# Optimization experiments

Hardware: AMD Instinct MI355X
Metric: run time of the kernel (lower is better)

## Reference

```python
import jax, jax.numpy as jnp
import numpy as np

N_HEAD = 16
SPARSE_TOPK = 64
NEG_INF = float('-inf')


def setup_inputs() -> dict:
    key = jax.random.key(0)
    ks = jax.random.split(key, 12)
    B, T, C = 4, 1024, 1024
    s = 0.02
    q = jax.random.normal(ks[0], (B, T, C), jnp.float32)
    kv = jax.random.normal(ks[1], (B, T, C), jnp.float32)  # forward asserts k == v
    tgt_mask = jnp.tril(jnp.ones((T, T), jnp.bool_)).reshape(1, 1, T, T)
    inp = {'q': q, 'k': kv, 'v': kv, 'tgt_mask': tgt_mask}
    for i, n in enumerate(['Wq', 'Wk', 'Wv', 'Wo']):
        inp[n] = jax.random.normal(ks[2 + i], (C, C), jnp.float32) * s
    for i, n in enumerate(['bq', 'bk', 'bv', 'bo']):
        inp[n] = jax.random.normal(ks[6 + i], (C,), jnp.float32) * s
    return inp


def reference(q, k, v, tgt_mask, Wq, Wk, Wv, Wo, bq, bk, bv, bo):
    B, T, C = q.shape
    H = N_HEAD
    hd = C // H
    scale = 1.0 / np.sqrt(hd).astype(np.float32)
    # QKV projections -> [B, H, T, hd]
    qh = (q @ Wq + bq).reshape(B, T, H, hd).transpose(0, 2, 1, 3)
    kh = (k @ Wk + bk).reshape(B, T, H, hd).transpose(0, 2, 1, 3)
    vh = (v @ Wv + bv).reshape(B, T, H, hd).transpose(0, 2, 1, 3)
    # full attention scores [B, H, T, T]
    att = jnp.einsum('bhtd,bhsd->bhts', qh, kh) * scale
    # causal mask: masked_fill where tgt_mask == 0
    att = jnp.where(tgt_mask[:, :, :T, :T], att, NEG_INF)
    # top-k sparse pruning: keep entries >= k-th largest per row (ties kept)
    top, _ = jax.lax.top_k(att, SPARSE_TOPK)
    vk = top[..., -1:]  # [B, H, T, 1]
    att = jnp.where(att < vk, NEG_INF, att)
    att = jax.nn.softmax(att, axis=-1)
    # dropout is identity in eval (p=0.0)
    y = jnp.einsum('bhts,bhsd->bhtd', att, vh)
    y = y.transpose(0, 2, 1, 3).reshape(B, T, C)
    return y @ Wo + bo
```

## Files before the change

kernel.cpp:

```cpp
#include <hip/hip_runtime.h>
#include <hip/hip_bf16.h>
#include <math.h>

typedef __attribute__((ext_vector_type(8))) short short8;
typedef __attribute__((ext_vector_type(4))) float f32x4;
typedef __attribute__((ext_vector_type(4))) int int4v;

#define SCL 0.1803368801111204f

static __device__ __forceinline__ unsigned short f2bf(float f) {
  unsigned u = __float_as_uint(f);
  u = u + 0x7FFFu + ((u >> 16) & 1u);
  return (unsigned short)(u >> 16);
}
static __device__ __forceinline__ unsigned pack2(float lo, float hi) {
  const unsigned ul = __float_as_uint(lo) + 0x8000u;
  const unsigned uh = __float_as_uint(hi) + 0x8000u;
  return (uh & 0xFFFF0000u) | (ul >> 16);
}

static __device__ __forceinline__ unsigned keyof(float x) {
  unsigned u = __float_as_uint(x);
  return (u & 0x80000000u) ? ~u : (u | 0x80000000u);
}
static __device__ __forceinline__ float keyinv(unsigned k) {
  unsigned u = (k & 0x80000000u) ? (k & 0x7FFFFFFFu) : ~k;
  return __uint_as_float(u);
}

static __device__ __forceinline__ int saddr(int r, int cc) {
  return (((r << 9) + cc) << 2) ^ ((r & 7) << 4);
}
static __device__ __forceinline__ int paddr(int r, int c) {
  return ((r << 11) + (c << 1)) ^ ((r & 7) << 4);
}

static __device__ __forceinline__ void gld_lds16(const unsigned short* g, unsigned short* l) {
  __builtin_amdgcn_global_load_lds(
      (const __attribute__((address_space(1))) void*)g,
      (__attribute__((address_space(3))) void*)l, 16, 0, 0);
}

__global__ __launch_bounds__(256) void wtrans4_k(const float* __restrict__ Wq,
                                                 const float* __restrict__ Wk,
                                                 const float* __restrict__ Wv,
                                                 const float* __restrict__ Wo,
                                                 unsigned short* __restrict__ Wqt,
                                                 unsigned short* __restrict__ Wkt,
                                                 unsigned short* __restrict__ Wvt,
                                                 unsigned short* __restrict__ Wot) {
  const int z = blockIdx.z;
  const float* W = (z == 0) ? Wq : (z == 1) ? Wk : (z == 2) ? Wv : Wo;
  unsigned short* Wt = (z == 0) ? Wqt : (z == 1) ? Wkt : (z == 2) ? Wvt : Wot;
  __shared__ float tile[32][33];
  const int tx = threadIdx.x, ty = threadIdx.y;
  const int x0 = blockIdx.x * 32, y0 = blockIdx.y * 32;
#pragma unroll
  for (int j = 0; j < 4; ++j)
    tile[ty + j * 8][tx] = W[(y0 + ty + j * 8) * 1024 + x0 + tx];
  __syncthreads();
#pragma unroll
  for (int j = 0; j < 4; ++j)
    Wt[(x0 + ty + j * 8) * 1024 + (y0 + tx)] = f2bf(tile[tx][ty + j * 8]);
}

template <int MODE>
static __device__ __forceinline__ void gemm_bodyF(unsigned short* As0, unsigned short* Bs0,
                                                  unsigned short* As1, unsigned short* Bs1,
                                                  const float* __restrict__ A,
                                                  const unsigned short* __restrict__ Bt,
                                                  const float* __restrict__ bias,
                                                  void* __restrict__ out) {
  const int tid = threadIdx.x;
  const int lane = tid & 63, w = tid >> 6;
  const int wr = w >> 1, wc = w & 1;
  const int m0 = blockIdx.y * 128, n0 = blockIdx.x * 128;
  const int l15 = lane & 15, l4 = lane >> 4;
  f32x4 acc[4][4] = {};
  const int r0 = tid >> 2, s0 = (tid & 3) * 8;
  const int r1 = r0 + 64;
  const float* gA0 = A + (m0 + r0) * 1024 + s0;
  const float* gA1 = A + (m0 + r1) * 1024 + s0;
  const unsigned short* gB0 = Bt + (n0 + r0) * 1024 + s0;
  const unsigned short* gB1 = Bt + (n0 + r1) * 1024 + s0;
  const int oA0 = r0 * 32 + s0, oA1 = r1 * 32 + s0;

  {
    const f32x4 a0 = *(const f32x4*)(gA0);
    const f32x4 a1 = *(const f32x4*)(gA0 + 4);
    const f32x4 c0 = *(const f32x4*)(gA1);
    const f32x4 c1 = *(const f32x4*)(gA1 + 4);
    gld_lds16(gB0, Bs0 + oA0);
    gld_lds16(gB1, Bs0 + oA1);
    int4v pa, pb;
    pa[0] = (int)pack2(a0[0], a0[1]); pa[1] = (int)pack2(a0[2], a0[3]);
    pa[2] = (int)pack2(a1[0], a1[1]); pa[3] = (int)pack2(a1[2], a1[3]);
    pb[0] = (int)pack2(c0[0], c0[1]); pb[1] = (int)pack2(c0[2], c0[3]);
    pb[2] = (int)pack2(c1[0], c1[1]); pb[3] = (int)pack2(c1[2], c1[3]);
    *(int4v*)(As0 + oA0) = pa;
    *(int4v*)(As0 + oA1) = pb;
  }
  __syncthreads();

  for (int kt = 0; kt < 32; ++kt) {
    f32x4 a0, a1, c0, c1;
    if (kt < 31) {
      const int k0n = (kt + 1) * 32;
      a0 = *(const f32x4*)(gA0 + k0n);
      a1 = *(const f32x4*)(gA0 + k0n + 4);
      c0 = *(const f32x4*)(gA1 + k0n);
      c1 = *(const f32x4*)(gA1 + k0n + 4);
      unsigned short* Bsn = (kt & 1) ? Bs0 : Bs1;
      gld_lds16(gB0 + k0n, Bsn + oA0);
      gld_lds16(gB1 + k0n, Bsn + oA1);
    }
    const unsigned short* Asc = (kt & 1) ? As1 : As0;
    const unsigned short* Bsc = (kt & 1) ? Bs1 : Bs0;
    short8 af[4], bfr[4];
#pragma unroll
    for (int i = 0; i < 4; ++i) {
      af[i]  = *(const short8*)(Asc + (wr * 64 + i * 16 + l15) * 32 + l4 * 8);
      bfr[i] = *(const short8*)(Bsc + (wc * 64 + i * 16 + l15) * 32 + l4 * 8);
    }
#pragma unroll
    for (int i = 0; i < 4; ++i)
#pragma unroll
      for (int j = 0; j < 4; ++j)
        acc[i][j] = __builtin_amdgcn_mfma_f32_16x16x32_bf16(af[i], bfr[j], acc[i][j], 0, 0, 0);
    if (kt < 31) {
      unsigned short* Asn = (kt & 1) ? As0 : As1;
      int4v pa, pb;
      pa[0] = (int)pack2(a0[0], a0[1]); pa[1] = (int)pack2(a0[2], a0[3]);
      pa[2] = (int)pack2(a1[0], a1[1]); pa[3] = (int)pack2(a1[2], a1[3]);
      pb[0] = (int)pack2(c0[0], c0[1]); pb[1] = (int)pack2(c0[2], c0[3]);
      pb[2] = (int)pack2(c1[0], c1[1]); pb[3] = (int)pack2(c1[2], c1[3]);
      *(int4v*)(Asn + oA0) = pa;
      *(int4v*)(Asn + oA1) = pb;
    }
    __syncthreads();
  }
#pragma unroll
  for (int i = 0; i < 4; ++i) {
#pragma unroll
    for (int j = 0; j < 4; ++j) {
      const int n = n0 + wc * 64 + j * 16 + l15;
      const float bv = bias[n];
#pragma unroll
      for (int r = 0; r < 4; ++r) {
        const int m = m0 + wr * 64 + i * 16 + l4 * 4 + r;
        const float v = acc[i][j][r] + bv;
        const int bb = m >> 10, t = m & 1023, hh = n >> 6, dd = n & 63;
        const unsigned short bfv = f2bf(v);
        if (MODE == 0)
          ((unsigned short*)out)[(((bb << 4) + hh) * 1024 + t) * 64 + dd] = bfv;
        else
          ((unsigned short*)out)[(((bb << 4) + hh) * 64 + dd) * 1024 + t] = bfv;
      }
    }
  }
}

__global__ __launch_bounds__(256) void gemm_qkv_k(
    const float* q, const float* k, const float* v,
    const unsigned short* Wqt, const unsigned short* Wkt, const unsigned short* Wvt,
    const float* bq, const float* bk, const float* bv,
    unsigned short* Qh, unsigned short* Kh, unsigned short* Vth) {
  __shared__ unsigned short As0[128 * 32], Bs0[128 * 32], As1[128 * 32], Bs1[128 * 32];
  const int z = blockIdx.z;
  const float* A           = (z == 0) ? q   : ((z == 1) ? k   : v);
  const unsigned short* Bt = (z == 0) ? Wqt : ((z == 1) ? Wkt : Wvt);
  const float* bias        = (z == 0) ? bq  : ((z == 1) ? bk  : bv);
  if (z == 2) gemm_bodyF<1>(As0, Bs0, As1, Bs1, A, Bt, bias, Vth);
  else        gemm_bodyF<0>(As0, Bs0, As1, Bs1, A, Bt, bias, z ? Kh : Qh);
}

__global__ __launch_bounds__(256) void gemm_out_k(const unsigned short* __restrict__ Y,
                                                  const unsigned short* __restrict__ Wot,
                                                  const float* __restrict__ bo,
                                                  float* __restrict__ out) {
  __shared__ unsigned short As0[128 * 32], Bs0[128 * 32], As1[128 * 32], Bs1[128 * 32];
  const int tid = threadIdx.x;
  const int lane = tid & 63, w = tid >> 6;
  const int wr = w >> 1, wc = w & 1;
  const int m0 = blockIdx.y * 128, n0 = blockIdx.x * 128;
  const int l15 = lane & 15, l4 = lane >> 4;
  f32x4 acc[4][4] = {};
  const int r0 = tid >> 2, s0 = (tid & 3) * 8;
  const int r1 = r0 + 64;
  const unsigned short* gA0 = Y + (m0 + r0) * 1024 + s0;
  const unsigned short* gA1 = Y + (m0 + r1) * 1024 + s0;
  const unsigned short* gB0 = Wot + (n0 + r0) * 1024 + s0;
  const unsigned short* gB1 = Wot + (n0 + r1) * 1024 + s0;
  const int oA0 = r0 * 32 + s0, oA1 = r1 * 32 + s0;

  gld_lds16(gA0, As0 + oA0);
  gld_lds16(gA1, As0 + oA1);
  gld_lds16(gB0, Bs0 + oA0);
  gld_lds16(gB1, Bs0 + oA1);
  __syncthreads();

  for (int kt = 0; kt < 32; ++kt) {
    if (kt < 31) {
      const int k0n = (kt + 1) * 32;
      unsigned short* Asn = (kt & 1) ? As0 : As1;
      unsigned short* Bsn = (kt & 1) ? Bs0 : Bs1;
      gld_lds16(gA0 + k0n, Asn + oA0);
      gld_lds16(gA1 + k0n, Asn + oA1);
      gld_lds16(gB0 + k0n, Bsn + oA0);
      gld_lds16(gB1 + k0n, Bsn + oA1);
    }
    const unsigned short* Asc = (kt & 1) ? As1 : As0;
    const unsigned short* Bsc = (kt & 1) ? Bs1 : Bs0;
    short8 af[4], bfr[4];
#pragma unroll
    for (int i = 0; i < 4; ++i) {
      af[i]  = *(const short8*)(Asc + (wr * 64 + i * 16 + l15) * 32 + l4 * 8);
      bfr[i] = *(const short8*)(Bsc + (wc * 64 + i * 16 + l15) * 32 + l4 * 8);
    }
#pragma unroll
    for (int i = 0; i < 4; ++i)
#pragma unroll
      for (int j = 0; j < 4; ++j)
        acc[i][j] = __builtin_amdgcn_mfma_f32_16x16x32_bf16(af[i], bfr[j], acc[i][j], 0, 0, 0);
    __syncthreads();
  }
#pragma unroll
  for (int i = 0; i < 4; ++i) {
#pragma unroll
    for (int j = 0; j < 4; ++j) {
      const int n = n0 + wc * 64 + j * 16 + l15;
      const float bv = bo[n];
#pragma unroll
      for (int r = 0; r < 4; ++r) {
        const int m = m0 + wr * 64 + i * 16 + l4 * 4 + r;
        out[m * 1024 + n] = acc[i][j][r] + bv;
      }
    }
  }
}

template <int NVAL, bool FORCE>
static __device__ __forceinline__ void process_row(char* __restrict__ smem, float (&v)[NVAL],
                                                   const int r, const int Lr, const int Lpad,
                                                   const int lane, float* __restrict__ RED2) {
  float lm = v[0];
#pragma unroll
  for (int i = 1; i < NVAL; ++i) lm = fmaxf(lm, v[i]);
  float mx = lm;
#pragma unroll
  for (int o = 32; o; o >>= 1) mx = fmaxf(mx, __shfl_xor(mx, o));

  float thr = -INFINITY;
  if (FORCE || Lr > 64) {
    float mn = lm;
#pragma unroll
    for (int o = 32; o; o >>= 1) mn = fminf(mn, __shfl_xor(mn, o));
    unsigned lo = (unsigned)__builtin_amdgcn_readfirstlane((int)keyof(mn));
    unsigned hi = (unsigned)__builtin_amdgcn_readfirstlane((int)keyof(mx)) + 1u;
    int cl = Lr, ch = 0, alt = 0;
    while (hi - lo > 1u) {
      const unsigned span = hi - lo;
      unsigned off;
      if (alt) off = span >> 1;
      else {
        const float fr = (float)(cl - 64) / (float)(cl - ch);
        off = (unsigned)(fr * (float)span);
        if (off < 1u) off = 1u;
        if (off > span - 1u) off = span - 1u;
      }
      alt ^= 1;
      const unsigned mid = lo + off;
      const float tm = keyinv(mid);
      int cnt = 0;
#pragma unroll
      for (int i = 0; i < NVAL; ++i) cnt += (int)__popcll(__ballot(v[i] >= tm));
      if (cnt >= 64) { lo = mid; cl = cnt; if (cnt == 64) break; }
      else { hi = mid; ch = cnt; }
    }
    thr = keyinv(lo);
  }

  float s = 0.f;
  unsigned pk[NVAL / 2];
#pragma unroll
  for (int p = 0; p < NVAL / 2; ++p) {
    const float p0 = (v[2 * p]     >= thr) ? exp2f(v[2 * p]     - mx) : 0.f;
    const float p1 = (v[2 * p + 1] >= thr) ? exp2f(v[2 * p + 1] - mx) : 0.f;
    s += p0 + p1;
    pk[p] = (unsigned)f2bf(p0) | ((unsigned)f2bf(p1) << 16);
  }
#pragma unroll
  for (int o = 32; o; o >>= 1) s += __shfl_xor(s, o);
  if (lane == 0) RED2[r] = 1.f / s;
#pragma unroll
  for (int p = 0; p < NVAL / 2; ++p) {
    const int c = ((p & 3) << 7) + (lane << 1) + ((p >= 4) ? 512 : 0);
    if (c < Lpad) *(unsigned*)(smem + paddr(r, c)) = pk[p];
  }
}

static __device__ __forceinline__ void pv_phase(char* __restrict__ smem,
                                                const unsigned short* __restrict__ Vh,
                                                unsigned short* __restrict__ Y,
                                                const int t0, const int h, const int b,
                                                const int lane, const int w, const int Lpad) {
  const int l15 = lane & 15, l4 = lane >> 4;
  float* RED  = (float*)(smem + 32768);
  float* RED2 = (float*)(smem + 32768 + 4352);
  const int nST = Lpad >> 5;
  const int stMid = (nST + 1) >> 1;
  const int d0 = (w & 3) * 16;
  const int stLo = (w < 4) ? 0 : stMid;
  const int stHi = (w < 4) ? stMid : nST;
  f32x4 acc = {0.f, 0.f, 0.f, 0.f};
  for (int st = stLo; st < stHi; ++st) {
    const int sb = st * 32 + l4 * 8;
    const short8 paf = *(const short8*)(smem + paddr(l15, sb));
    const short8 vb = *(const short8*)(Vh + (d0 + l15) * 1024 + sb);
    acc = __builtin_amdgcn_mfma_f32_16x16x32_bf16(paf, vb, acc, 0, 0, 0);
  }
  if (w >= 4) {
    const int base = (w - 4) * 272 + l15;
#pragma unroll
    for (int r = 0; r < 4; ++r) RED[base + (l4 * 4 + r) * 17] = acc[r];
  }
  __syncthreads();
  if (w < 4) {
    const int base = w * 272 + l15;
    const int d = (h << 6) + d0 + l15;
#pragma unroll
    for (int r = 0; r < 4; ++r) {
      const float inv = RED2[l4 * 4 + r];
      const float vr = (acc[r] + RED[base + (l4 * 4 + r) * 17]) * inv;
      const int tg = t0 + l4 * 4 + r;
      Y[((b << 10) + tg) * 1024 + d] = f2bf(vr);
    }
  }
}

__global__ __launch_bounds__(512, 6) void attn_hv_k(const unsigned short* __restrict__ Q,
                                                    const unsigned short* __restrict__ K,
                                                    const unsigned short* __restrict__ Vt,
                                                    unsigned short* __restrict__ Y) {
  extern __shared__ __align__(16) char smem[];
  const int tid = threadIdx.x, lane = tid & 63, w = tid >> 6;
  const int t0 = 1008 - 16 * (int)blockIdx.x;
  const int h = blockIdx.y, b = blockIdx.z;
  const unsigned short* Qp = Q + (((b * 16 + h) * 1024) + t0) * 64;
  const unsigned short* Kh = K + (b * 16 + h) * 65536;
  const unsigned short* Vh = Vt + (b * 16 + h) * 65536;
  const int L = t0 + 16;
  const int Lpad = (L + 31) & ~31;
  const int nCT = L >> 4;
  const int l15 = lane & 15, l4 = lane >> 4;
  float* RED2 = (float*)(smem + 32768 + 4352);

  const short8 aq0 = *(const short8*)(Qp + l15 * 64 + l4 * 8);
  const short8 aq1 = *(const short8*)(Qp + l15 * 64 + 32 + l4 * 8);

  auto qk_chunk = [&](int tlo, int thi) {
    for (int ct = tlo + w; ct < thi; ct += 8) {
      const int c0 = ct * 16;
      const short8 kb0 = *(const short8*)(Kh + (c0 + l15) * 64 + l4 * 8);
      const short8 kb1 = *(const short8*)(Kh + (c0 + l15) * 64 + 32 + l4 * 8);
      f32x4 acc = {0.f, 0.f, 0.f, 0.f};
      acc = __builtin_amdgcn_mfma_f32_16x16x32_bf16(aq0, kb0, acc, 0, 0, 0);
      acc = __builtin_amdgcn_mfma_f32_16x16x32_bf16(aq1, kb1, acc, 0, 0, 0);
      const int c = c0 + l15, cc = c & 511;
      if (ct == nCT - 1) {
#pragma unroll
        for (int r = 0; r < 4; ++r) {
          const int row = l4 * 4 + r;
          *(float*)(smem + saddr(row, cc)) = (c <= t0 + row) ? acc[r] * SCL : -INFINITY;
        }
      } else {
#pragma unroll
        for (int r = 0; r < 4; ++r)
          *(float*)(smem + saddr(l4 * 4 + r, cc)) = acc[r] * SCL;
      }
    }
  };

  qk_chunk(0, 32);
  __syncthreads();
  const int rA = w * 2, rB = rA + 1;
  const int LrA = t0 + rA + 1, LrB = t0 + rB + 1;
  float vA[16], vB[16];
#pragma unroll
  for (int p = 0; p < 4; ++p) {
    const int c = (p << 7) + (lane << 1);
    const float2 tA = *(const float2*)(smem + saddr(rA, c));
    const float2 tB = *(const float2*)(smem + saddr(rB, c));
    vA[2 * p] = tA.x; vA[2 * p + 1] = tA.y;
    vB[2 * p] = tB.x; vB[2 * p + 1] = tB.y;
  }
  __syncthreads();
  qk_chunk(32, nCT);
  __syncthreads();
#pragma unroll
  for (int p = 0; p < 4; ++p) {
    const int cc = (p << 7) + (lane << 1);
    const float2 tA = *(const float2*)(smem + saddr(rA, cc));
    const bool vld = (cc + 512) < L;
    vA[8 + 2 * p] = vld ? tA.x : -INFINITY;
    vA[9 + 2 * p] = vld ? tA.y : -INFINITY;
  }
  process_row<16, true>(smem, vA, rA, LrA, Lpad, lane, RED2);
#pragma unroll
  for (int p = 0; p < 4; ++p) {
    const int cc = (p << 7) + (lane << 1);
    const float2 tB = *(const float2*)(smem + saddr(rB, cc));
    const bool vld = (cc + 512) < L;
    vB[8 + 2 * p] = vld ? tB.x : -INFINITY;
    vB[9 + 2 * p] = vld ? tB.y : -INFINITY;
  }
  process_row<16, true>(smem, vB, rB, LrB, Lpad, lane, RED2);
  __syncthreads();
  pv_phase(smem, Vh, Y, t0, h, b, lane, w, Lpad);
}

__global__ __launch_bounds__(512, 6) void attn_lt_k(const unsigned short* __restrict__ Q,
                                                    const unsigned short* __restrict__ K,
                                                    const unsigned short* __restrict__ Vt,
                                                    unsigned short* __restrict__ Y) {
  extern __shared__ __align__(16) char smem[];
  const int tid = threadIdx.x, lane = tid & 63, w = tid >> 6;
  const int t0 = 496 - 16 * (int)blockIdx.x;
  const int h = blockIdx.y, b = blockIdx.z;
  const unsigned short* Qp = Q + (((b * 16 + h) * 1024) + t0) * 64;
  const unsigned short* Kh = K + (b * 16 + h) * 65536;
  const unsigned short* Vh = Vt + (b * 16 + h) * 65536;
  const int L = t0 + 16;
  const int Lpad = (L + 31) & ~31;
  const int nCT = L >> 4;
  const int l15 = lane & 15, l4 = lane >> 4;
  float* RED2 = (float*)(smem + 32768 + 4352);

  const short8 aq0 = *(const short8*)(Qp + l15 * 64 + l4 * 8);
  const short8 aq1 = *(const short8*)(Qp + l15 * 64 + 32 + l4 * 8);

  for (int ct = w; ct < nCT; ct += 8) {
    const int c0 = ct * 16;
    const short8 kb0 = *(const short8*)(Kh + (c0 + l15) * 64 + l4 * 8);
    const short8 kb1 = *(const short8*)(Kh + (c0 + l15) * 64 + 32 + l4 * 8);
    f32x4 acc = {0.f, 0.f, 0.f, 0.f};
    acc = __builtin_amdgcn_mfma_f32_16x16x32_bf16(aq0, kb0, acc, 0, 0, 0);
    acc = __builtin_amdgcn_mfma_f32_16x16x32_bf16(aq1, kb1, acc, 0, 0, 0);
    const int c = c0 + l15, cc = c & 511;
    if (ct == nCT - 1) {
#pragma unroll
      for (int r = 0; r < 4; ++r) {
        const int row = l4 * 4 + r;
        *(float*)(smem + saddr(row, cc)) = (c <= t0 + row) ? acc[r] * SCL : -INFINITY;
      }
    } else {
#pragma unroll
      for (int r = 0; r < 4; ++r)
        *(float*)(smem + saddr(l4 * 4 + r, cc)) = acc[r] * SCL;
    }
  }
  __syncthreads();

  const int rA = w * 2, rB = rA + 1;
  const int LrA = t0 + rA + 1, LrB = t0 + rB + 1;
  float vA[8], vB[8];
#pragma unroll
  for (int p = 0; p < 4; ++p) {
    const int c = (p << 7) + (lane << 1);
    const float2 tA = *(const float2*)(smem + saddr(rA, c));
    const float2 tB = *(const float2*)(smem + saddr(rB, c));
    const bool vld = c < L;
    vA[2 * p]     = vld ? tA.x : -INFINITY;
    vA[2 * p + 1] = vld ? tA.y : -INFINITY;
    vB[2 * p]     = vld ? tB.x : -INFINITY;
    vB[2 * p + 1] = vld ? tB.y : -INFINITY;
  }
  process_row<8, false>(smem, vA, rA, LrA, Lpad, lane, RED2);
  process_row<8, false>(smem, vB, rB, LrB, Lpad, lane, RED2);
  __syncthreads();
  pv_phase(smem, Vh, Y, t0, h, b, lane, w, Lpad);
}

extern "C" void kernel_launch(void* const* d_in, const int* in_sizes, int n_in,
                              void* d_out, int out_size, void* d_ws, size_t ws_size,
                              hipStream_t stream) {
  const float* q  = (const float*)d_in[0];
  const float* k  = (const float*)d_in[1];
  const float* v  = (const float*)d_in[2];
  const float* Wq = (const float*)d_in[4];
  const float* Wk = (const float*)d_in[5];
  const float* Wv = (const float*)d_in[6];
  const float* Wo = (const float*)d_in[7];
  const float* bq = (const float*)d_in[8];
  const float* bk = (const float*)d_in[9];
  const float* bv = (const float*)d_in[10];
  const float* bo = (const float*)d_in[11];

  char* ws = (char*)d_ws;
  const size_t MB = 1u << 20;
  unsigned short* Y   = (unsigned short*)(ws + 0 * MB);
  unsigned short* Wqt = (unsigned short*)(ws + 24 * MB);
  unsigned short* Wkt = (unsigned short*)(ws + 26 * MB);
  unsigned short* Wvt = (unsigned short*)(ws + 28 * MB);
  unsigned short* Wot = (unsigned short*)(ws + 30 * MB);
  unsigned short* Qh  = (unsigned short*)(ws + 32 * MB);
  unsigned short* Kh  = (unsigned short*)(ws + 40 * MB);
  unsigned short* Vth = (unsigned short*)(ws + 48 * MB);

  wtrans4_k<<<dim3(32, 32, 4), dim3(32, 8), 0, stream>>>(Wq, Wk, Wv, Wo, Wqt, Wkt, Wvt, Wot);
  gemm_qkv_k<<<dim3(8, 32, 3), 256, 0, stream>>>(q, k, v, Wqt, Wkt, Wvt,
                                                 bq, bk, bv, Qh, Kh, Vth);
  attn_hv_k<<<dim3(32, 16, 4), 512, 37248, stream>>>(Qh, Kh, Vth, Y);
  attn_lt_k<<<dim3(32, 16, 4), 512, 37248, stream>>>(Qh, Kh, Vth, Y);
  gemm_out_k<<<dim3(8, 32), 256, 0, stream>>>(Y, Wot, bo, (float*)d_out);
}
```

Before: 223.6 us.

## Double attention block size to 16 waves, one query row per wave

Both attention kernels now launch 1024 threads instead of 512. Each of the 16 waves handles one query row in the top-k/softmax phase instead of two. The PV phase splits the key dimension four ways instead of two, combining partial sums through a larger shared-memory reduction buffer. The goal is to cut the serial per-wave work in the row-processing and PV phases. In exchange it uses more shared memory per block and more barrier overhead, and the new launch bounds may limit registers and occupancy.

```diff
diff --git a/kernel.cpp b/kernel.cpp
--- a/kernel.cpp
+++ b/kernel.cpp
@@ -299,49 +299,51 @@
   }
 }
 
-static __device__ __forceinline__ void pv_phase(char* __restrict__ smem,
-                                                const unsigned short* __restrict__ Vh,
-                                                unsigned short* __restrict__ Y,
-                                                const int t0, const int h, const int b,
-                                                const int lane, const int w, const int Lpad) {
+static __device__ __forceinline__ void pv_phase16(char* __restrict__ smem,
+                                                  const unsigned short* __restrict__ Vh,
+                                                  unsigned short* __restrict__ Y,
+                                                  const int t0, const int h, const int b,
+                                                  const int lane, const int w, const int Lpad) {
   const int l15 = lane & 15, l4 = lane >> 4;
-  float* RED  = (float*)(smem + 32768);
-  float* RED2 = (float*)(smem + 32768 + 4352);
+  float* RED3 = (float*)(smem + 32768);
+  float* RED2 = (float*)(smem + 32768 + 13056);
   const int nST = Lpad >> 5;
-  const int stMid = (nST + 1) >> 1;
+  const int q = (nST + 3) >> 2;
+  const int kseg = w >> 2;
   const int d0 = (w & 3) * 16;
-  const int stLo = (w < 4) ? 0 : stMid;
-  const int stHi = (w < 4) ? stMid : nST;
+  int lo = kseg * q, hi = lo + q;
+  if (lo > nST) lo = nST;
+  if (hi > nST) hi = nST;
   f32x4 acc = {0.f, 0.f, 0.f, 0.f};
-  for (int st = stLo; st < stHi; ++st) {
+  for (int st = lo; st < hi; ++st) {
     const int sb = st * 32 + l4 * 8;
     const short8 paf = *(const short8*)(smem + paddr(l15, sb));
     const short8 vb = *(const short8*)(Vh + (d0 + l15) * 1024 + sb);
     acc = __builtin_amdgcn_mfma_f32_16x16x32_bf16(paf, vb, acc, 0, 0, 0);
   }
-  if (w >= 4) {
-    const int base = (w - 4) * 272 + l15;
-#pragma unroll
-    for (int r = 0; r < 4; ++r) RED[base + (l4 * 4 + r) * 17] = acc[r];
-  }
-  __syncthreads();
-  if (w < 4) {
-    const int base = w * 272 + l15;
+  if (kseg > 0) {
+#pragma unroll
+    for (int r = 0; r < 4; ++r)
+      RED3[((kseg - 1) * 16 + l4 * 4 + r) * 68 + d0 + l15] = acc[r];
+  }
+  __syncthreads();
+  if (kseg == 0) {
     const int d = (h << 6) + d0 + l15;
 #pragma unroll
     for (int r = 0; r < 4; ++r) {
-      const float inv = RED2[l4 * 4 + r];
-      const float vr = (acc[r] + RED[base + (l4 * 4 + r) * 17]) * inv;
-      const int tg = t0 + l4 * 4 + r;
-      Y[((b << 10) + tg) * 1024 + d] = f2bf(vr);
-    }
-  }
-}
-
-__global__ __launch_bounds__(512, 6) void attn_hv_k(const unsigned short* __restrict__ Q,
-                                                    const unsigned short* __restrict__ K,
-                                                    const unsigned short* __restrict__ Vt,
-                                                    unsigned short* __restrict__ Y) {
+      const int row = l4 * 4 + r;
+      const int col = d0 + l15;
+      float s = acc[r] + RED3[(row) * 68 + col] + RED3[(16 + row) * 68 + col] +
+                RED3[(32 + row) * 68 + col];
+      Y[((b << 10) + t0 + row) * 1024 + d] = f2bf(s * RED2[row]);
+    }
+  }
+}
+
+__global__ __launch_bounds__(1024, 8) void attn_hv_k(const unsigned short* __restrict__ Q,
+                                                     const unsigned short* __restrict__ K,
+                                                     const unsigned short* __restrict__ Vt,
+                                                     unsigned short* __restrict__ Y) {
   extern __shared__ __align__(16) char smem[];
   const int tid = threadIdx.x, lane = tid & 63, w = tid >> 6;
   const int t0 = 1008 - 16 * (int)blockIdx.x;
@@ -353,13 +355,13 @@
   const int Lpad = (L + 31) & ~31;
   const int nCT = L >> 4;
   const int l15 = lane & 15, l4 = lane >> 4;
-  float* RED2 = (float*)(smem + 32768 + 4352);
+  float* RED2 = (float*)(smem + 32768 + 13056);
 
   const short8 aq0 = *(const short8*)(Qp + l15 * 64 + l4 * 8);
   const short8 aq1 = *(const short8*)(Qp + l15 * 64 + 32 + l4 * 8);
 
   auto qk_chunk = [&](int tlo, int thi) {
-    for (int ct = tlo + w; ct < thi; ct += 8) {
+    for (int ct = tlo + w; ct < thi; ct += 16) {
       const int c0 = ct * 16;
       const short8 kb0 = *(const short8*)(Kh + (c0 + l15) * 64 + l4 * 8);
       const short8 kb1 = *(const short8*)(Kh + (c0 + l15) * 64 + 32 + l4 * 8);
@@ -383,16 +385,13 @@
 
   qk_chunk(0, 32);
   __syncthreads();
-  const int rA = w * 2, rB = rA + 1;
-  const int LrA = t0 + rA + 1, LrB = t0 + rB + 1;
-  float vA[16], vB[16];
+  const int Lr = t0 + w + 1;
+  float v[16];
 #pragma unroll
   for (int p = 0; p < 4; ++p) {
     const int c = (p << 7) + (lane << 1);
-    const float2 tA = *(const float2*)(smem + saddr(rA, c));
-    const float2 tB = *(const float2*)(smem + saddr(rB, c));
-    vA[2 * p] = tA.x; vA[2 * p + 1] = tA.y;
-    vB[2 * p] = tB.x; vB[2 * p + 1] = tB.y;
+    const float2 t = *(const float2*)(smem + saddr(w, c));
+    v[2 * p] = t.x; v[2 * p + 1] = t.y;
   }
   __syncthreads();
   qk_chunk(32, nCT);
@@ -400,29 +399,20 @@
 #pragma unroll
   for (int p = 0; p < 4; ++p) {
     const int cc = (p << 7) + (lane << 1);
-    const float2 tA = *(const float2*)(smem + saddr(rA, cc));
+    const float2 t = *(const float2*)(smem + saddr(w, cc));
     const bool vld = (cc + 512) < L;
-    vA[8 + 2 * p] = vld ? tA.x : -INFINITY;
-    vA[9 + 2 * p] = vld ? tA.y : -INFINITY;
-  }
-  process_row<16, true>(smem, vA, rA, LrA, Lpad, lane, RED2);
-#pragma unroll
-  for (int p = 0; p < 4; ++p) {
-    const int cc = (p << 7) + (lane << 1);
-    const float2 tB = *(const float2*)(smem + saddr(rB, cc));
-    const bool vld = (cc + 512) < L;
-    vB[8 + 2 * p] = vld ? tB.x : -INFINITY;
-    vB[9 + 2 * p] = vld ? tB.y : -INFINITY;
-  }
-  process_row<16, true>(smem, vB, rB, LrB, Lpad, lane, RED2);
-  __syncthreads();
-  pv_phase(smem, Vh, Y, t0, h, b, lane, w, Lpad);
-}
-
-__global__ __launch_bounds__(512, 6) void attn_lt_k(const unsigned short* __restrict__ Q,
-                                                    const unsigned short* __restrict__ K,
-                                                    const unsigned short* __restrict__ Vt,
-                                                    unsigned short* __restrict__ Y) {
+    v[8 + 2 * p] = vld ? t.x : -INFINITY;
+    v[9 + 2 * p] = vld ? t.y : -INFINITY;
+  }
+  process_row<16, true>(smem, v, w, Lr, Lpad, lane, RED2);
+  __syncthreads();
+  pv_phase16(smem, Vh, Y, t0, h, b, lane, w, Lpad);
+}
+
+__global__ __launch_bounds__(1024, 8) void attn_lt_k(const unsigned short* __restrict__ Q,
+                                                     const unsigned short* __restrict__ K,
+                                                     const unsigned short* __restrict__ Vt,
+                                                     unsigned short* __restrict__ Y) {
   extern __shared__ __align__(16) char smem[];
   const int tid = threadIdx.x, lane = tid & 63, w = tid >> 6;
   const int t0 = 496 - 16 * (int)blockIdx.x;
@@ -434,12 +424,12 @@
   const int Lpad = (L + 31) & ~31;
   const int nCT = L >> 4;
   const int l15 = lane & 15, l4 = lane >> 4;
-  float* RED2 = (float*)(smem + 32768 + 4352);
+  float* RED2 = (float*)(smem + 32768 + 13056);
 
   const short8 aq0 = *(const short8*)(Qp + l15 * 64 + l4 * 8);
   const short8 aq1 = *(const short8*)(Qp + l15 * 64 + 32 + l4 * 8);
 
-  for (int ct = w; ct < nCT; ct += 8) {
+  for (int ct = w; ct < nCT; ct += 16) {
     const int c0 = ct * 16;
     const short8 kb0 = *(const short8*)(Kh + (c0 + l15) * 64 + l4 * 8);
     const short8 kb1 = *(const short8*)(Kh + (c0 + l15) * 64 + 32 + l4 * 8);
@@ -461,24 +451,19 @@
   }
   __syncthreads();
 
-  const int rA = w * 2, rB = rA + 1;
-  const int LrA = t0 + rA + 1, LrB = t0 + rB + 1;
-  float vA[8], vB[8];
+  const int Lr = t0 + w + 1;
+  float v[8];
 #pragma unroll
   for (int p = 0; p < 4; ++p) {
     const int c = (p << 7) + (lane << 1);
-    const float2 tA = *(const float2*)(smem + saddr(rA, c));
-    const float2 tB = *(const float2*)(smem + saddr(rB, c));
+    const float2 t = *(const float2*)(smem + saddr(w, c));
     const bool vld = c < L;
-    vA[2 * p]     = vld ? tA.x : -INFINITY;
-    vA[2 * p + 1] = vld ? tA.y : -INFINITY;
-    vB[2 * p]     = vld ? tB.x : -INFINITY;
-    vB[2 * p + 1] = vld ? tB.y : -INFINITY;
-  }
-  process_row<8, false>(smem, vA, rA, LrA, Lpad, lane, RED2);
-  process_row<8, false>(smem, vB, rB, LrB, Lpad, lane, RED2);
-  __syncthreads();
-  pv_phase(smem, Vh, Y, t0, h, b, lane, w, Lpad);
+    v[2 * p]     = vld ? t.x : -INFINITY;
+    v[2 * p + 1] = vld ? t.y : -INFINITY;
+  }
+  process_row<8, false>(smem, v, w, Lr, Lpad, lane, RED2);
+  __syncthreads();
+  pv_phase16(smem, Vh, Y, t0, h, b, lane, w, Lpad);
 }
 
 extern "C" void kernel_launch(void* const* d_in, const int* in_sizes, int n_in,
@@ -510,7 +495,7 @@
   wtrans4_k<<<dim3(32, 32, 4), dim3(32, 8), 0, stream>>>(Wq, Wk, Wv, Wo, Wqt, Wkt, Wvt, Wot);
   gemm_qkv_k<<<dim3(8, 32, 3), 256, 0, stream>>>(q, k, v, Wqt, Wkt, Wvt,
                                                  bq, bk, bv, Qh, Kh, Vth);
-  attn_hv_k<<<dim3(32, 16, 4), 512, 37248, stream>>>(Qh, Kh, Vth, Y);
-  attn_lt_k<<<dim3(32, 16, 4), 512, 37248, stream>>>(Qh, Kh, Vth, Y);
+  attn_hv_k<<<dim3(32, 16, 4), 1024, 45888, stream>>>(Qh, Kh, Vth, Y);
+  attn_lt_k<<<dim3(32, 16, 4), 1024, 45888, stream>>>(Qh, Kh, Vth, Y);
   gemm_out_k<<<dim3(8, 32), 256, 0, stream>>>(Y, Wot, bo, (float*)d_out);
 }
```

Measured after the change: 231.9 us. 3.7% more time.
